# Performance work log

Measured on AMD Instinct MI355X. Metric: run time of the kernel, lower is better.

## Reference

```python
import jax, jax.numpy as jnp
import numpy as np

B, C, H, W = 32, 512, 64, 64
K = 32  # num_codes


def setup_inputs() -> dict:
    key = jax.random.key(0)
    k1, k2, k3 = jax.random.split(key, 3)
    x = jax.random.normal(k1, (B, C, H, W), dtype=jnp.float32)
    std = 1.0 / (K * C) ** 0.5
    codewords = jax.random.uniform(k2, (K, C), dtype=jnp.float32, minval=-std, maxval=std)
    scale = jax.random.uniform(k3, (K,), dtype=jnp.float32, minval=-1.0, maxval=0.0)
    return {"x": x, "codewords": codewords, "scale": scale}


def reference(x, codewords, scale):
    # x: [B, C, H, W] -> [B, N, C] with N = H*W
    b, c = x.shape[0], x.shape[1]
    xf = x.reshape(b, c, -1).transpose(0, 2, 1)  # [B, N, C]
    # scaled L2: scale_k * ||x_n - c_k||^2, expanded algebraically to avoid [B,N,K,C]
    x2 = jnp.sum(xf * xf, axis=-1)                      # [B, N]
    c2 = jnp.sum(codewords * codewords, axis=-1)        # [K]
    xc = jnp.einsum('bnc,kc->bnk', xf, codewords)       # [B, N, K]
    dist = scale[None, None, :] * (x2[:, :, None] - 2.0 * xc + c2[None, None, :])
    w = jax.nn.softmax(dist, axis=2)                    # [B, N, K]
    # aggregate: sum_n w_{nk} * (x_n - c_k) = (w^T x) - (sum_n w_{nk}) * c_k
    wx = jnp.einsum('bnk,bnc->bkc', w, xf)              # [B, K, C]
    wsum = jnp.sum(w, axis=1)                           # [B, K]
    encoded_feat = wx - wsum[:, :, None] * codewords[None, :, :]  # [B, K, C]
    return encoded_feat
```

## Files before the change

kernel.cpp:

```cpp
#include <hip/hip_runtime.h>
#include <stdint.h>

#define Bdim 32
#define Cdim 512
#define Ndim 4096
#define Kdim 32
#define NPX 32
#define NCH 16
#define PWIN 8

static constexpr size_t WS_WSUM_OFF = (size_t)256 * Kdim * Cdim * 4;
static constexpr size_t WS_C2_OFF   = WS_WSUM_OFF + (size_t)256 * Kdim * 4;

using bf16x8 = __attribute__((ext_vector_type(8))) short;
using f32x4  = __attribute__((ext_vector_type(4))) float;

static __device__ __forceinline__ unsigned short f2bf(float f) {
    unsigned int u = __float_as_uint(f);
    u += 0x7fffu + ((u >> 16) & 1u);
    return (unsigned short)(u >> 16);
}

__global__ __launch_bounds__(256) void k0_c2(const float* __restrict__ cw,
                                             float* __restrict__ c2) {
    __shared__ float partl[8][32];
    int t = threadIdx.x;
    int k = t & 31, g = t >> 5;
    float s = 0.f;
    int c0 = g * 64;
    for (int c = c0; c < c0 + 64; ++c) {
        float v = cw[k * Cdim + c];
        s += v * v;
    }
    partl[g][k] = s;
    __syncthreads();
    if (t < 32) {
        float tot = 0.f;
        #pragma unroll
        for (int gg = 0; gg < 8; ++gg) tot += partl[gg][t];
        c2[t] = tot;
    }
}

__global__ __launch_bounds__(512, 2) void k1_fused(const float* __restrict__ x,
                                                   const float* __restrict__ cw,
                                                   const float* __restrict__ scale,
                                                   const float* __restrict__ c2g,
                                                   float* __restrict__ part,
                                                   float* __restrict__ wsum_part) {
    __shared__ unsigned short cw_s[Kdim][520];
    __shared__ unsigned short x_n[NPX][520];
    __shared__ unsigned short x_t[Cdim][40];
    __shared__ float          S_s[2][NPX][36];
    __shared__ unsigned short w_t[Kdim][40];
    __shared__ float          x2_w[8][NPX];
    __shared__ float          wsum_w[4][Kdim];

    const int t    = threadIdx.x;
    const int blk  = blockIdx.x;
    const int b    = blk >> 3;
    const int pw   = blk & 7;
    const int lane = t & 63;
    const int lr   = lane & 15;
    const int lq   = lane >> 4;
    const int wv   = t >> 6;
    const int pp   = t & 15;
    const int crg  = t >> 4;
    const int q    = t & 7;
    const int px   = t >> 3;
    const int pt   = wv & 1;
    const int kt2  = (wv >> 1) & 1;
    const int ch   = wv >> 2;

    #pragma unroll
    for (int i = 0; i < 8; ++i) {
        int f4 = t + 512 * i;
        int k  = f4 >> 7;
        int c4 = (f4 & 127) * 4;
        float4 v = *(const float4*)(cw + (size_t)k * Cdim + c4);
        ushort4 u;
        u.x = f2bf(v.x); u.y = f2bf(v.y); u.z = f2bf(v.z); u.w = f2bf(v.w);
        *(ushort4*)&cw_s[k][c4] = u;
    }

    float4 sc4, c24;
    if (t < 256) {
        sc4 = *(const float4*)(scale + 4 * q);
        c24 = *(const float4*)(c2g + 4 * q);
    }

    const float* xb = x + (size_t)b * Cdim * Ndim;

    float2 pa[8], pb[8];
    {
        int n0 = pw * 512;
        #pragma unroll
        for (int i = 0; i < 8; ++i) {
            int c = 2 * crg + 64 * i;
            pa[i] = *(const float2*)(xb + (size_t)c * Ndim + n0 + 2 * pp);
            pb[i] = *(const float2*)(xb + (size_t)(c + 1) * Ndim + n0 + 2 * pp);
        }
    }

    f32x4 acc[2][4];
    #pragma unroll
    for (int kt = 0; kt < 2; ++kt)
        #pragma unroll
        for (int ct = 0; ct < 4; ++ct) acc[kt][ct] = (f32x4){0.f, 0.f, 0.f, 0.f};
    float wsum_r[4] = {0.f, 0.f, 0.f, 0.f};

    __syncthreads();

    for (int ci = 0; ci < NCH; ++ci) {
        float x2p0 = 0.f, x2p1 = 0.f;
        #pragma unroll
        for (int i = 0; i < 8; ++i) {
            int c = 2 * crg + 64 * i;
            float2 a = pa[i], bb = pb[i];
            unsigned short ax = f2bf(a.x), ay = f2bf(a.y);
            unsigned short bx = f2bf(bb.x), by = f2bf(bb.y);
            ushort2 u;
            u.x = ax; u.y = ay; *(ushort2*)&x_t[c][2 * pp] = u;
            u.x = bx; u.y = by; *(ushort2*)&x_t[c + 1][2 * pp] = u;
            u.x = ax; u.y = bx; *(ushort2*)&x_n[2 * pp][c] = u;
            u.x = ay; u.y = by; *(ushort2*)&x_n[2 * pp + 1][c] = u;
            x2p0 += a.x * a.x + bb.x * bb.x;
            x2p1 += a.y * a.y + bb.y * bb.y;
        }
        x2p0 += __shfl_xor(x2p0, 16); x2p1 += __shfl_xor(x2p1, 16);
        x2p0 += __shfl_xor(x2p0, 32); x2p1 += __shfl_xor(x2p1, 32);
        if (lane < 16) {
            float2 v; v.x = x2p0; v.y = x2p1;
            *(float2*)&x2_w[wv][2 * pp] = v;
        }
        if (ci + 1 < NCH) {
            int nn = pw * 512 + (ci + 1) * 32;
            #pragma unroll
            for (int i = 0; i < 8; ++i) {
                int c = 2 * crg + 64 * i;
                pa[i] = *(const float2*)(xb + (size_t)c * Ndim + nn + 2 * pp);
                pb[i] = *(const float2*)(xb + (size_t)(c + 1) * Ndim + nn + 2 * pp);
            }
        }
        __syncthreads();

        {
            f32x4 d = (f32x4){0.f, 0.f, 0.f, 0.f};
            #pragma unroll
            for (int s = 0; s < 8; ++s) {
                int col = 256 * ch + 32 * s + 8 * lq;
                bf16x8 av = *(const bf16x8*)&x_n[16 * pt + lr][col];
                bf16x8 bv = *(const bf16x8*)&cw_s[16 * kt2 + lr][col];
                d = __builtin_amdgcn_mfma_f32_16x16x32_bf16(av, bv, d, 0, 0, 0);
            }
            #pragma unroll
            for (int r = 0; r < 4; ++r)
                S_s[ch][16 * pt + 4 * lq + r][16 * kt2 + lr] = d[r];
        }
        __syncthreads();

        if (t < 256) {
            float4 dv0 = *(const float4*)&S_s[0][px][4 * q];
            float4 dv1 = *(const float4*)&S_s[1][px][4 * q];
            float xx = 0.f;
            #pragma unroll
            for (int w = 0; w < 8; ++w) xx += x2_w[w][px];
            float d0 = sc4.x * (xx - 2.f * (dv0.x + dv1.x) + c24.x);
            float d1 = sc4.y * (xx - 2.f * (dv0.y + dv1.y) + c24.y);
            float d2 = sc4.z * (xx - 2.f * (dv0.z + dv1.z) + c24.z);
            float d3 = sc4.w * (xx - 2.f * (dv0.w + dv1.w) + c24.w);
            float m = fmaxf(fmaxf(d0, d1), fmaxf(d2, d3));
            m = fmaxf(m, __shfl_xor(m, 1));
            m = fmaxf(m, __shfl_xor(m, 2));
            m = fmaxf(m, __shfl_xor(m, 4));
            float e0 = __expf(d0 - m), e1 = __expf(d1 - m);
            float e2 = __expf(d2 - m), e3 = __expf(d3 - m);
            float ss = e0 + e1 + e2 + e3;
            ss += __shfl_xor(ss, 1);
            ss += __shfl_xor(ss, 2);
            ss += __shfl_xor(ss, 4);
            float inv = 1.f / ss;
            float w0 = e0 * inv, w1 = e1 * inv, w2 = e2 * inv, w3 = e3 * inv;
            wsum_r[0] += w0; wsum_r[1] += w1; wsum_r[2] += w2; wsum_r[3] += w3;
            w_t[4 * q + 0][px] = f2bf(w0);
            w_t[4 * q + 1][px] = f2bf(w1);
            w_t[4 * q + 2][px] = f2bf(w2);
            w_t[4 * q + 3][px] = f2bf(w3);
        }
        __syncthreads();

        {
            bf16x8 a0 = *(const bf16x8*)&w_t[lr][8 * lq];
            bf16x8 a1 = *(const bf16x8*)&w_t[16 + lr][8 * lq];
            #pragma unroll
            for (int ct = 0; ct < 4; ++ct) {
                bf16x8 bv = *(const bf16x8*)&x_t[64 * wv + 16 * ct + lr][8 * lq];
                acc[0][ct] = __builtin_amdgcn_mfma_f32_16x16x32_bf16(a0, bv, acc[0][ct], 0, 0, 0);
                acc[1][ct] = __builtin_amdgcn_mfma_f32_16x16x32_bf16(a1, bv, acc[1][ct], 0, 0, 0);
            }
        }
        __syncthreads();
    }

    if (t < 256) {
        #pragma unroll
        for (int j = 0; j < 4; ++j) {
            float v = wsum_r[j];
            v += __shfl_xor(v, 8);
            v += __shfl_xor(v, 16);
            v += __shfl_xor(v, 32);
            if (lane < 8) wsum_w[wv][4 * lane + j] = v;
        }
    }
    {
        float* pbuf = part + (size_t)blk * (Kdim * Cdim);
        #pragma unroll
        for (int kt = 0; kt < 2; ++kt)
            #pragma unroll
            for (int ct = 0; ct < 4; ++ct)
                #pragma unroll
                for (int r = 0; r < 4; ++r)
                    pbuf[(size_t)(16 * kt + 4 * lq + r) * Cdim + 64 * wv + 16 * ct + lr] =
                        acc[kt][ct][r];
    }
    __syncthreads();
    if (t < 32) {
        float s = wsum_w[0][t] + wsum_w[1][t] + wsum_w[2][t] + wsum_w[3][t];
        wsum_part[blk * Kdim + t] = s;
    }
}

__global__ __launch_bounds__(256) void k2_reduce(const float* __restrict__ part,
                                                 const float* __restrict__ wsum_part,
                                                 const float* __restrict__ cw,
                                                 float* __restrict__ out) {
    int blk = blockIdx.x;
    int b = blk >> 5, k = blk & 31;
    int t = threadIdx.x;
    float ws = 0.f;
    #pragma unroll
    for (int p = 0; p < PWIN; ++p) ws += wsum_part[(b * PWIN + p) * Kdim + k];
    int c = 2 * t;
    float sx = 0.f, sy = 0.f;
    #pragma unroll
    for (int p = 0; p < PWIN; ++p) {
        const float2 v = *(const float2*)(part + ((size_t)(b * PWIN + p) * Kdim + k) * Cdim + c);
        sx += v.x;
        sy += v.y;
    }
    float2 cv = *(const float2*)(cw + (size_t)k * Cdim + c);
    float2 o;
    o.x = sx - ws * cv.x;
    o.y = sy - ws * cv.y;
    *(float2*)(out + ((size_t)b * Kdim + k) * Cdim + c) = o;
}

extern "C" void kernel_launch(void* const* d_in, const int* in_sizes, int n_in,
                              void* d_out, int out_size, void* d_ws, size_t ws_size,
                              hipStream_t stream) {
    const float* x     = (const float*)d_in[0];
    const float* cw    = (const float*)d_in[1];
    const float* scale = (const float*)d_in[2];
    float* out = (float*)d_out;

    char* wsb = (char*)d_ws;
    float* part      = (float*)wsb;
    float* wsum_part = (float*)(wsb + WS_WSUM_OFF);
    float* c2        = (float*)(wsb + WS_C2_OFF);

    k0_c2<<<1, 256, 0, stream>>>(cw, c2);
    k1_fused<<<Bdim * PWIN, 512, 0, stream>>>(x, cw, scale, c2, part, wsum_part);
    k2_reduce<<<Bdim * Kdim, 256, 0, stream>>>(part, wsum_part, cw, out);
}
```

Before: 381.9 us.

## Store x once in a tiled LDS layout with transpose reads, double the grid

Replaces the two bf16 copies of each x chunk (pixel-major and channel-major) with a single tiled layout. The first GEMM reads it through ds_read_b64_tr_b16 transpose loads, and the aggregation GEMM reads it directly. The grid doubles to 16 pixel windows per batch with half as many chunks each, and launch bounds now ask for 4 blocks per CU because LDS use is lower. It also switches to the packed v_cvt_pk_bf16_f32 conversion and splits the first GEMM across two accumulators. The cost is twice as many partial results for the reduction stage, plus inline asm with an explicit lgkmcnt(0) wait that may serialize LDS reads.

```diff
diff --git a/kernel.cpp b/kernel.cpp
--- a/kernel.cpp
+++ b/kernel.cpp
@@ -6,19 +6,30 @@
 #define Ndim 4096
 #define Kdim 32
 #define NPX 32
-#define NCH 16
-#define PWIN 8
-
-static constexpr size_t WS_WSUM_OFF = (size_t)256 * Kdim * Cdim * 4;
-static constexpr size_t WS_C2_OFF   = WS_WSUM_OFF + (size_t)256 * Kdim * 4;
+#define NCH 8
+#define PWIN 16
+
+static constexpr size_t WS_WSUM_OFF = (size_t)512 * Kdim * Cdim * 4;
+static constexpr size_t WS_C2_OFF   = WS_WSUM_OFF + (size_t)512 * Kdim * 4;
 
 using bf16x8 = __attribute__((ext_vector_type(8))) short;
+using s16x4  = __attribute__((ext_vector_type(4))) short;
 using f32x4  = __attribute__((ext_vector_type(4))) float;
 
 static __device__ __forceinline__ unsigned short f2bf(float f) {
     unsigned int u = __float_as_uint(f);
     u += 0x7fffu + ((u >> 16) & 1u);
     return (unsigned short)(u >> 16);
+}
+
+static __device__ __forceinline__ unsigned int cvtpk(float lo, float hi) {
+    unsigned int r;
+    asm("v_cvt_pk_bf16_f32 %0, %1, %2" : "=v"(r) : "v"(lo), "v"(hi));
+    return r;
+}
+
+static __device__ __forceinline__ uint32_t lds_addr(const void* p) {
+    return (uint32_t)(uintptr_t)p;
 }
 
 __global__ __launch_bounds__(256) void k0_c2(const float* __restrict__ cw,
@@ -42,15 +53,14 @@
     }
 }
 
-__global__ __launch_bounds__(512, 2) void k1_fused(const float* __restrict__ x,
+__global__ __launch_bounds__(512, 4) void k1_fused(const float* __restrict__ x,
                                                    const float* __restrict__ cw,
                                                    const float* __restrict__ scale,
                                                    const float* __restrict__ c2g,
                                                    float* __restrict__ part,
                                                    float* __restrict__ wsum_part) {
-    __shared__ unsigned short cw_s[Kdim][520];
-    __shared__ unsigned short x_n[NPX][520];
-    __shared__ unsigned short x_t[Cdim][40];
+    __shared__ __align__(16) unsigned short xt2[64 * 272];
+    __shared__ unsigned short cw_s[Kdim][516];
     __shared__ float          S_s[2][NPX][36];
     __shared__ unsigned short w_t[Kdim][40];
     __shared__ float          x2_w[8][NPX];
@@ -58,8 +68,8 @@
 
     const int t    = threadIdx.x;
     const int blk  = blockIdx.x;
-    const int b    = blk >> 3;
-    const int pw   = blk & 7;
+    const int b    = blk >> 4;
+    const int pw   = blk & 15;
     const int lane = t & 63;
     const int lr   = lane & 15;
     const int lq   = lane >> 4;
@@ -78,9 +88,10 @@
         int k  = f4 >> 7;
         int c4 = (f4 & 127) * 4;
         float4 v = *(const float4*)(cw + (size_t)k * Cdim + c4);
-        ushort4 u;
-        u.x = f2bf(v.x); u.y = f2bf(v.y); u.z = f2bf(v.z); u.w = f2bf(v.w);
-        *(ushort4*)&cw_s[k][c4] = u;
+        uint2 uu;
+        uu.x = cvtpk(v.x, v.y);
+        uu.y = cvtpk(v.z, v.w);
+        *(uint2*)&cw_s[k][c4] = uu;
     }
 
     float4 sc4, c24;
@@ -93,7 +104,7 @@
 
     float2 pa[8], pb[8];
     {
-        int n0 = pw * 512;
+        int n0 = pw * 256;
         #pragma unroll
         for (int i = 0; i < 8; ++i) {
             int c = 2 * crg + 64 * i;
@@ -117,13 +128,10 @@
         for (int i = 0; i < 8; ++i) {
             int c = 2 * crg + 64 * i;
             float2 a = pa[i], bb = pb[i];
-            unsigned short ax = f2bf(a.x), ay = f2bf(a.y);
-            unsigned short bx = f2bf(bb.x), by = f2bf(bb.y);
-            ushort2 u;
-            u.x = ax; u.y = ay; *(ushort2*)&x_t[c][2 * pp] = u;
-            u.x = bx; u.y = by; *(ushort2*)&x_t[c + 1][2 * pp] = u;
-            u.x = ax; u.y = bx; *(ushort2*)&x_n[2 * pp][c] = u;
-            u.x = ay; u.y = by; *(ushort2*)&x_n[2 * pp + 1][c] = u;
+            int T   = 2 * (c >> 4) + (pp >> 3);
+            int ush = T * 272 + (c & 15) * 16 + 2 * (pp & 7);
+            *(unsigned int*)&xt2[ush]      = cvtpk(a.x, a.y);
+            *(unsigned int*)&xt2[ush + 16] = cvtpk(bb.x, bb.y);
             x2p0 += a.x * a.x + bb.x * bb.x;
             x2p1 += a.y * a.y + bb.y * bb.y;
         }
@@ -134,7 +142,7 @@
             *(float2*)&x2_w[wv][2 * pp] = v;
         }
         if (ci + 1 < NCH) {
-            int nn = pw * 512 + (ci + 1) * 32;
+            int nn = pw * 256 + (ci + 1) * 32;
             #pragma unroll
             for (int i = 0; i < 8; ++i) {
                 int c = 2 * crg + 64 * i;
@@ -145,17 +153,32 @@
         __syncthreads();
 
         {
-            f32x4 d = (f32x4){0.f, 0.f, 0.f, 0.f};
+            f32x4 d0 = (f32x4){0.f, 0.f, 0.f, 0.f};
+            f32x4 d1 = (f32x4){0.f, 0.f, 0.f, 0.f};
+            const int kr = 16 * kt2 + lr;
+            const uint32_t trbase = lds_addr(xt2) +
+                (uint32_t)((32 * ch + pt) * 544 + 128 * (lane >> 4) + 2 * (lane & 15));
             #pragma unroll
             for (int s = 0; s < 8; ++s) {
-                int col = 256 * ch + 32 * s + 8 * lq;
-                bf16x8 av = *(const bf16x8*)&x_n[16 * pt + lr][col];
-                bf16x8 bv = *(const bf16x8*)&cw_s[16 * kt2 + lr][col];
-                d = __builtin_amdgcn_mfma_f32_16x16x32_bf16(av, bv, d, 0, 0, 0);
+                s16x4 xlo, xhi;
+                uint32_t a0 = trbase + (uint32_t)(s * 4 * 544);
+                asm volatile("ds_read_b64_tr_b16 %0, %2\n\t"
+                             "ds_read_b64_tr_b16 %1, %3\n\t"
+                             "s_waitcnt lgkmcnt(0)"
+                             : "=&v"(xlo), "=&v"(xhi)
+                             : "v"(a0), "v"(a0 + 1088u));
+                const int c0 = 256 * ch + 32 * s + 4 * lq;
+                s16x4 blo = *(const s16x4*)&cw_s[kr][c0];
+                s16x4 bhi = *(const s16x4*)&cw_s[kr][c0 + 16];
+                bf16x8 av = __builtin_shufflevector(xlo, xhi, 0, 1, 2, 3, 4, 5, 6, 7);
+                bf16x8 bv = __builtin_shufflevector(blo, bhi, 0, 1, 2, 3, 4, 5, 6, 7);
+                if (s & 1) d1 = __builtin_amdgcn_mfma_f32_16x16x32_bf16(av, bv, d1, 0, 0, 0);
+                else       d0 = __builtin_amdgcn_mfma_f32_16x16x32_bf16(av, bv, d0, 0, 0, 0);
             }
+            d0 += d1;
             #pragma unroll
             for (int r = 0; r < 4; ++r)
-                S_s[ch][16 * pt + 4 * lq + r][16 * kt2 + lr] = d[r];
+                S_s[ch][16 * pt + 4 * lq + r][16 * kt2 + lr] = d0[r];
         }
         __syncthreads();
 
@@ -194,7 +217,8 @@
             bf16x8 a1 = *(const bf16x8*)&w_t[16 + lr][8 * lq];
             #pragma unroll
             for (int ct = 0; ct < 4; ++ct) {
-                bf16x8 bv = *(const bf16x8*)&x_t[64 * wv + 16 * ct + lr][8 * lq];
+                int T = 2 * (4 * wv + ct) + (lq >> 1);
+                bf16x8 bv = *(const bf16x8*)&xt2[T * 272 + lr * 16 + 8 * (lq & 1)];
                 acc[0][ct] = __builtin_amdgcn_mfma_f32_16x16x32_bf16(a0, bv, acc[0][ct], 0, 0, 0);
                 acc[1][ct] = __builtin_amdgcn_mfma_f32_16x16x32_bf16(a1, bv, acc[1][ct], 0, 0, 0);
             }
```

After: 384.3 us. No clear change (+0.6%).
